# Kernel tuning notes

Measured on AMD Instinct MI355X. Metric: run time of the kernel, lower is better.

The kernel has to match this reference:

```python
import jax, jax.numpy as jnp
import numpy as np

IN_F = 4096
OUT_F = 4096
BATCH = 8192


def setup_inputs() -> dict:
    key = jax.random.key(0)
    ks = jax.random.split(key, 7)
    bound = 1.0 / np.sqrt(IN_F)
    return {
        "x": jax.random.normal(ks[0], (BATCH, IN_F), dtype=jnp.float32),
        "weight_mu": jax.random.normal(ks[1], (OUT_F, IN_F), dtype=jnp.float32) * np.sqrt(2.0 / IN_F),  # kaiming fan_in relu
        "weight_log_var": jnp.full((OUT_F, IN_F), -6.0, dtype=jnp.float32),
        "bias_mu": jax.random.uniform(ks[2], (OUT_F,), dtype=jnp.float32, minval=-bound, maxval=bound),
        "bias_log_var": jnp.full((OUT_F,), -6.0, dtype=jnp.float32),
        "weight_eps": jax.random.normal(ks[3], (OUT_F, IN_F), dtype=jnp.float32),
        "bias_eps": jax.random.normal(ks[4], (OUT_F,), dtype=jnp.float32),
    }


def reference(x, weight_mu, weight_log_var, bias_mu, bias_log_var, weight_eps, bias_eps):
    # Reparameterized sampling: w = mu + eps * exp(0.5 * log_var)
    weight = weight_mu + weight_eps * jnp.exp(0.5 * weight_log_var)   # [out, in]
    bias = bias_mu + bias_eps * jnp.exp(0.5 * bias_log_var)           # [out]
    # F.linear(x, weight, bias) = x @ weight.T + bias
    return jnp.einsum("bi,oi->bo", x, weight) + bias
```

## Files before the change

kernel.cpp:

```cpp
#include <hip/hip_runtime.h>
#include <hip/hip_bf16.h>
#include <stdint.h>

typedef __bf16 bf16x8 __attribute__((ext_vector_type(8)));
typedef float f32x4 __attribute__((ext_vector_type(4)));

__device__ inline unsigned short f2bf_rne(float f) {
  unsigned int u = __float_as_uint(f);
  u += 0x7fffu + ((u >> 16) & 1u);
  return (unsigned short)(u >> 16);
}

__global__ __launch_bounds__(256) void prep_weight(
    const float* __restrict__ mu, const float* __restrict__ lv,
    const float* __restrict__ eps, unsigned short* __restrict__ wbf, int n4) {
  int i = blockIdx.x * 256 + threadIdx.x;
  if (i >= n4) return;
  float4 m = ((const float4*)mu)[i];
  float4 v = ((const float4*)lv)[i];
  float4 e = ((const float4*)eps)[i];
  ushort4 p;
  p.x = f2bf_rne(m.x + e.x * __expf(0.5f * v.x));
  p.y = f2bf_rne(m.y + e.y * __expf(0.5f * v.y));
  p.z = f2bf_rne(m.z + e.z * __expf(0.5f * v.z));
  p.w = f2bf_rne(m.w + e.w * __expf(0.5f * v.w));
  ((ushort4*)wbf)[i] = p;
}

__global__ __launch_bounds__(256) void prep_x(
    const float* __restrict__ x, unsigned short* __restrict__ xbf, int n4) {
  int i = blockIdx.x * 256 + threadIdx.x;
  if (i >= n4) return;
  float4 m = ((const float4*)x)[i];
  ushort4 p;
  p.x = f2bf_rne(m.x);
  p.y = f2bf_rne(m.y);
  p.z = f2bf_rne(m.z);
  p.w = f2bf_rne(m.w);
  ((ushort4*)xbf)[i] = p;
}

#define BM 128
#define BN 128
#define BK 64

__global__ __launch_bounds__(256) void gemm_bt_bias(
    const unsigned short* __restrict__ A,
    const unsigned short* __restrict__ B,
    const float* __restrict__ bmu, const float* __restrict__ blv,
    const float* __restrict__ beps,
    float* __restrict__ C, int M, int N, int K) {
  __shared__ __align__(16) unsigned short As[BM * BK];
  __shared__ __align__(16) unsigned short Bs[BN * BK];

  const int tid  = threadIdx.x;
  const int wave = tid >> 6;
  const int lane = tid & 63;
  const int wm = wave >> 1;
  const int wn = wave & 1;

  const int rowA0 = blockIdx.y * BM;
  const int rowB0 = blockIdx.x * BN;

  const int srow = tid >> 3;
  const int scol = (tid & 7) * 8;

  f32x4 acc[4][4];
#pragma unroll
  for (int i = 0; i < 4; ++i)
#pragma unroll
    for (int j = 0; j < 4; ++j)
      acc[i][j] = (f32x4){0.f, 0.f, 0.f, 0.f};

  const int mrow = lane & 15;
  const int kgrp = (lane >> 4) * 8;

  for (int k0 = 0; k0 < K; k0 += BK) {
#pragma unroll
    for (int j = 0; j < 4; ++j) {
      const int r = j * 32 + srow;
      const unsigned short* gA = A + (size_t)(rowA0 + r) * K + k0 + scol;
      const unsigned short* gB = B + (size_t)(rowB0 + r) * K + k0 + scol;
      __builtin_amdgcn_global_load_lds(
          (const __attribute__((address_space(1))) unsigned int*)gA,
          (__attribute__((address_space(3))) unsigned int*)&As[(j * 256 + wave * 64) * 8],
          16, 0, 0);
      __builtin_amdgcn_global_load_lds(
          (const __attribute__((address_space(1))) unsigned int*)gB,
          (__attribute__((address_space(3))) unsigned int*)&Bs[(j * 256 + wave * 64) * 8],
          16, 0, 0);
    }
    __syncthreads();

#pragma unroll
    for (int kk = 0; kk < BK; kk += 32) {
      bf16x8 af[4], bfv[4];
#pragma unroll
      for (int mi = 0; mi < 4; ++mi)
        af[mi] = *(const bf16x8*)&As[(wm * 64 + mi * 16 + mrow) * BK + kk + kgrp];
#pragma unroll
      for (int ni = 0; ni < 4; ++ni)
        bfv[ni] = *(const bf16x8*)&Bs[(wn * 64 + ni * 16 + mrow) * BK + kk + kgrp];
#pragma unroll
      for (int mi = 0; mi < 4; ++mi)
#pragma unroll
        for (int ni = 0; ni < 4; ++ni)
          acc[mi][ni] = __builtin_amdgcn_mfma_f32_16x16x32_bf16(
              af[mi], bfv[ni], acc[mi][ni], 0, 0, 0);
    }
    __syncthreads();
  }

  const int colq = lane & 15;
  const int rq4  = (lane >> 4) * 4;
#pragma unroll
  for (int ni = 0; ni < 4; ++ni) {
    const int col = rowB0 + wn * 64 + ni * 16 + colq;
    const float bias = bmu[col] + beps[col] * __expf(0.5f * blv[col]);
#pragma unroll
    for (int mi = 0; mi < 4; ++mi) {
      const int rbase = rowA0 + wm * 64 + mi * 16 + rq4;
#pragma unroll
      for (int r = 0; r < 4; ++r)
        C[(size_t)(rbase + r) * N + col] = acc[mi][ni][r] + bias;
    }
  }
}

extern "C" void kernel_launch(void* const* d_in, const int* in_sizes, int n_in,
                              void* d_out, int out_size, void* d_ws, size_t ws_size,
                              hipStream_t stream) {
  const float* x    = (const float*)d_in[0];
  const float* wmu  = (const float*)d_in[1];
  const float* wlv  = (const float*)d_in[2];
  const float* bmu  = (const float*)d_in[3];
  const float* blv  = (const float*)d_in[4];
  const float* weps = (const float*)d_in[5];
  const float* beps = (const float*)d_in[6];
  float* out = (float*)d_out;

  const int M = 8192, N = 4096, K = 4096;

  unsigned short* xbf = (unsigned short*)d_ws;
  unsigned short* wbf = xbf + (size_t)M * K;

  const int n4w = N * K / 4;
  prep_weight<<<n4w / 256, 256, 0, stream>>>(wmu, wlv, weps, wbf, n4w);
  const int n4x = M * K / 4;
  prep_x<<<n4x / 256, 256, 0, stream>>>(x, xbf, n4x);

  dim3 grid(N / BN, M / BM);
  gemm_bt_bias<<<grid, 256, 0, stream>>>(xbf, wbf, bmu, blv, beps, out, M, N, K);
}
```

Measured before the change: 742.5 us.

## XOR-swizzle LDS tiles in GEMM and widen bf16 conversion kernels

The GEMM's global-to-LDS copy now permutes each 16-byte k-group within a row by XORing it with the row index. The MFMA fragment reads apply the same XOR to find their data, which spreads the 128-byte-strided row reads across LDS banks and is meant to cut bank conflicts. Separately, the weight-sampling and x-to-bf16 prep kernels now handle 8 elements per thread and issue 16-byte stores, halving the thread count. This adds some index arithmetic in the inner loop and relies on the swizzle matching exactly between the write and read sides.

```diff
diff --git a/kernel.cpp b/kernel.cpp
--- a/kernel.cpp
+++ b/kernel.cpp
@@ -4,6 +4,7 @@
 
 typedef __bf16 bf16x8 __attribute__((ext_vector_type(8)));
 typedef float f32x4 __attribute__((ext_vector_type(4)));
+typedef unsigned short u16x8 __attribute__((ext_vector_type(8)));
 
 __device__ inline unsigned short f2bf_rne(float f) {
   unsigned int u = __float_as_uint(f);
@@ -12,32 +13,36 @@
 }
 
 __global__ __launch_bounds__(256) void prep_weight(
-    const float* __restrict__ mu, const float* __restrict__ lv,
-    const float* __restrict__ eps, unsigned short* __restrict__ wbf, int n4) {
+    const float4* __restrict__ mu, const float4* __restrict__ lv,
+    const float4* __restrict__ eps, u16x8* __restrict__ wbf, int n8) {
   int i = blockIdx.x * 256 + threadIdx.x;
-  if (i >= n4) return;
-  float4 m = ((const float4*)mu)[i];
-  float4 v = ((const float4*)lv)[i];
-  float4 e = ((const float4*)eps)[i];
-  ushort4 p;
-  p.x = f2bf_rne(m.x + e.x * __expf(0.5f * v.x));
-  p.y = f2bf_rne(m.y + e.y * __expf(0.5f * v.y));
-  p.z = f2bf_rne(m.z + e.z * __expf(0.5f * v.z));
-  p.w = f2bf_rne(m.w + e.w * __expf(0.5f * v.w));
-  ((ushort4*)wbf)[i] = p;
+  if (i >= n8) return;
+  float4 m0 = mu[2 * i], m1 = mu[2 * i + 1];
+  float4 v0 = lv[2 * i], v1 = lv[2 * i + 1];
+  float4 e0 = eps[2 * i], e1 = eps[2 * i + 1];
+  u16x8 p;
+  p[0] = f2bf_rne(m0.x + e0.x * __expf(0.5f * v0.x));
+  p[1] = f2bf_rne(m0.y + e0.y * __expf(0.5f * v0.y));
+  p[2] = f2bf_rne(m0.z + e0.z * __expf(0.5f * v0.z));
+  p[3] = f2bf_rne(m0.w + e0.w * __expf(0.5f * v0.w));
+  p[4] = f2bf_rne(m1.x + e1.x * __expf(0.5f * v1.x));
+  p[5] = f2bf_rne(m1.y + e1.y * __expf(0.5f * v1.y));
+  p[6] = f2bf_rne(m1.z + e1.z * __expf(0.5f * v1.z));
+  p[7] = f2bf_rne(m1.w + e1.w * __expf(0.5f * v1.w));
+  wbf[i] = p;
 }
 
 __global__ __launch_bounds__(256) void prep_x(
-    const float* __restrict__ x, unsigned short* __restrict__ xbf, int n4) {
+    const float4* __restrict__ x, u16x8* __restrict__ xbf, int n8) {
   int i = blockIdx.x * 256 + threadIdx.x;
-  if (i >= n4) return;
-  float4 m = ((const float4*)x)[i];
-  ushort4 p;
-  p.x = f2bf_rne(m.x);
-  p.y = f2bf_rne(m.y);
-  p.z = f2bf_rne(m.z);
-  p.w = f2bf_rne(m.w);
-  ((ushort4*)xbf)[i] = p;
+  if (i >= n8) return;
+  float4 m0 = x[2 * i], m1 = x[2 * i + 1];
+  u16x8 p;
+  p[0] = f2bf_rne(m0.x); p[1] = f2bf_rne(m0.y);
+  p[2] = f2bf_rne(m0.z); p[3] = f2bf_rne(m0.w);
+  p[4] = f2bf_rne(m1.x); p[5] = f2bf_rne(m1.y);
+  p[6] = f2bf_rne(m1.z); p[7] = f2bf_rne(m1.w);
+  xbf[i] = p;
 }
 
 #define BM 128
@@ -63,7 +68,7 @@
   const int rowB0 = blockIdx.x * BN;
 
   const int srow = tid >> 3;
-  const int scol = (tid & 7) * 8;
+  const int scol = (((tid & 7) ^ ((tid >> 3) & 7))) * 8;
 
   f32x4 acc[4][4];
 #pragma unroll
@@ -73,7 +78,7 @@
       acc[i][j] = (f32x4){0.f, 0.f, 0.f, 0.f};
 
   const int mrow = lane & 15;
-  const int kgrp = (lane >> 4) * 8;
+  const int gsel = lane >> 4;
 
   for (int k0 = 0; k0 < K; k0 += BK) {
 #pragma unroll
@@ -96,11 +101,17 @@
     for (int kk = 0; kk < BK; kk += 32) {
       bf16x8 af[4], bfv[4];
 #pragma unroll
-      for (int mi = 0; mi < 4; ++mi)
-        af[mi] = *(const bf16x8*)&As[(wm * 64 + mi * 16 + mrow) * BK + kk + kgrp];
+      for (int mi = 0; mi < 4; ++mi) {
+        const int row = wm * 64 + mi * 16 + mrow;
+        const int pg = ((kk >> 3) + gsel) ^ (mrow & 7);
+        af[mi] = *(const bf16x8*)&As[row * BK + pg * 8];
+      }
 #pragma unroll
-      for (int ni = 0; ni < 4; ++ni)
-        bfv[ni] = *(const bf16x8*)&Bs[(wn * 64 + ni * 16 + mrow) * BK + kk + kgrp];
+      for (int ni = 0; ni < 4; ++ni) {
+        const int row = wn * 64 + ni * 16 + mrow;
+        const int pg = ((kk >> 3) + gsel) ^ (mrow & 7);
+        bfv[ni] = *(const bf16x8*)&Bs[row * BK + pg * 8];
+      }
 #pragma unroll
       for (int mi = 0; mi < 4; ++mi)
 #pragma unroll
@@ -144,10 +155,12 @@
   unsigned short* xbf = (unsigned short*)d_ws;
   unsigned short* wbf = xbf + (size_t)M * K;
 
-  const int n4w = N * K / 4;
-  prep_weight<<<n4w / 256, 256, 0, stream>>>(wmu, wlv, weps, wbf, n4w);
-  const int n4x = M * K / 4;
-  prep_x<<<n4x / 256, 256, 0, stream>>>(x, xbf, n4x);
+  const int n8w = N * K / 8;
+  prep_weight<<<n8w / 256, 256, 0, stream>>>(
+      (const float4*)wmu, (const float4*)wlv, (const float4*)weps,
+      (u16x8*)wbf, n8w);
+  const int n8x = M * K / 8;
+  prep_x<<<n8x / 256, 256, 0, stream>>>((const float4*)x, (u16x8*)xbf, n8x);
 
   dim3 grid(N / BN, M / BM);
   gemm_bt_bias<<<grid, 256, 0, stream>>>(xbf, wbf, bmu, blv, beps, out, M, N, K);
```

New measurement: 668.9 us. 9.9% less time.
